# Kernel optimization log

Measured on AMD Instinct MI355X. Metric: run time of the kernel, lower is better.

Reference implementation:

```python
import jax, jax.numpy as jnp
import numpy as np

NUM_ROUTING = 3

def _squash(s):
    # squared_norm * s / ((1 + squared_norm) * sqrt(squared_norm)), norm over last dim
    sn = jnp.sum(s * s, axis=-1, keepdims=True)
    return sn * s / ((1.0 + sn) * jnp.sqrt(sn))

def setup_inputs() -> dict:
    key = jax.random.key(0)
    kx, kw = jax.random.split(key)
    B, IN_CAPS, IN_DIM, OUT_CAPS, OUT_DIM = 64, 8192, 8, 8, 16
    x = jax.random.normal(kx, (B, IN_CAPS, IN_DIM), dtype=jnp.float32)
    W = 0.01 * jax.random.normal(kw, (IN_CAPS, OUT_CAPS, IN_DIM, OUT_DIM), dtype=jnp.float32)
    return {"x": x, "W": W}

def reference(x, W):
    # x: [B, in_caps, in_dim]; W: [in_caps, out_caps, in_dim, out_dim]
    u_hat = jnp.einsum('ijnm,bin->bijm', W, x)          # [B, i, j, m]
    temp_u_hat = jax.lax.stop_gradient(u_hat)           # detach, routing uses no grads
    B, I, J = x.shape[0], W.shape[0], W.shape[1]
    b = jnp.zeros((B, I, J), dtype=x.dtype)
    for _ in range(NUM_ROUTING - 1):
        c = jax.nn.softmax(b, axis=2)                   # over out_caps j
        s = jnp.einsum('bij,bijm->bjm', c, temp_u_hat)  # [B, j, m]
        v = _squash(s)
        b = b + jnp.einsum('bjm,bijm->bij', v, temp_u_hat)  # agreement
    c = jax.nn.softmax(b, axis=2)
    s = jnp.einsum('bij,bijm->bjm', c, u_hat)
    return _squash(s)                                   # [B, out_caps, out_dim]
```

## Files before the change

kernel.cpp:

```cpp
#include <hip/hip_runtime.h>


#define BB      64
#define ICAPS   8192
#define NDIM    8
#define JCAPS   8
#define MDIM    16
#define NBLK    256
#define ICHUNK  (ICAPS / NBLK)
#define IG      8
#define NSTAGE  (ICHUNK / IG)
#define JW      4
#define MW      4
#define WJ_STRIDE (NDIM * MDIM + 4)
#define WI_STRIDE (JCAPS * WJ_STRIDE)
#define S_ELEMS  (BB * JCAPS * MDIM)

template <int MODE>
__global__ __launch_bounds__(512, 1) void caps_pass_kernel(
    const float* __restrict__ x, const float* __restrict__ W,
    const float* __restrict__ vsum, float* __restrict__ partial)
{
    __shared__ float Wlds[IG * WI_STRIDE];

    const int tid = threadIdx.x;
    const int b   = tid >> 3;
    const int g   = tid & 7;
    const int jh  = g >> 2;
    const int mq  = g & 3;
    const int blk = blockIdx.x;
    const int i0  = blk * ICHUNK;

    float s_acc[JW][MW];
    #pragma unroll
    for (int a = 0; a < JW; ++a)
        #pragma unroll
        for (int c = 0; c < MW; ++c) s_acc[a][c] = 0.f;

    float vreg[JW][MW];
    if (MODE == 1) {
        #pragma unroll
        for (int jj = 0; jj < JW; ++jj) {
            const float4 vv = *(const float4*)&vsum[(b * JCAPS + jh * JW + jj) * MDIM + mq * 4];
            vreg[jj][0] = vv.x; vreg[jj][1] = vv.y; vreg[jj][2] = vv.z; vreg[jj][3] = vv.w;
        }
    }

    for (int st = 0; st < NSTAGE; ++st) {
        {
            const int iL  = tid >> 6;
            const int rem = tid & 63;
            const int j   = rem >> 3;
            const int n   = rem & 7;
            const float4* src = (const float4*)(W + (size_t)(i0 + st * IG + iL) * 1024
                                                  + j * 128 + n * 16);
            float4* dst = (float4*)&Wlds[iL * WI_STRIDE + j * WJ_STRIDE + n * 16];
            dst[0] = src[0]; dst[1] = src[1]; dst[2] = src[2]; dst[3] = src[3];
        }
        __syncthreads();

        #pragma unroll
        for (int ii = 0; ii < IG; ++ii) {
            const int i = i0 + st * IG + ii;
            const float4 xa = *(const float4*)&x[((size_t)b * ICAPS + i) * NDIM];
            const float4 xb = *(const float4*)&x[((size_t)b * ICAPS + i) * NDIM + 4];
            const float xs[8] = {xa.x, xa.y, xa.z, xa.w, xb.x, xb.y, xb.z, xb.w};

            float u[JW][MW] = {};
            const float* wbase = &Wlds[ii * WI_STRIDE + (jh * JW) * WJ_STRIDE + mq * 4];
            #pragma unroll
            for (int jj = 0; jj < JW; ++jj) {
                #pragma unroll
                for (int n = 0; n < NDIM; ++n) {
                    const float4 wq = *(const float4*)&wbase[jj * WJ_STRIDE + n * MDIM];
                    u[jj][0] += xs[n] * wq.x;
                    u[jj][1] += xs[n] * wq.y;
                    u[jj][2] += xs[n] * wq.z;
                    u[jj][3] += xs[n] * wq.w;
                }
            }

            if (MODE == 0) {
                #pragma unroll
                for (int jj = 0; jj < JW; ++jj)
                    #pragma unroll
                    for (int mm = 0; mm < MW; ++mm) s_acc[jj][mm] += u[jj][mm];
            } else {
                float lp[JW];
                #pragma unroll
                for (int jj = 0; jj < JW; ++jj)
                    lp[jj] = u[jj][0] * vreg[jj][0] + u[jj][1] * vreg[jj][1]
                           + u[jj][2] * vreg[jj][2] + u[jj][3] * vreg[jj][3];
                #pragma unroll
                for (int jj = 0; jj < JW; ++jj) {
                    lp[jj] += __shfl_xor(lp[jj], 1);
                    lp[jj] += __shfl_xor(lp[jj], 2);
                }
                float lo[JW];
                #pragma unroll
                for (int jj = 0; jj < JW; ++jj) lo[jj] = __shfl_xor(lp[jj], 4);
                float mx = lp[0];
                #pragma unroll
                for (int jj = 1; jj < JW; ++jj) mx = fmaxf(mx, lp[jj]);
                #pragma unroll
                for (int jj = 0; jj < JW; ++jj) mx = fmaxf(mx, lo[jj]);
                float e[JW];
                float den = 0.f;
                #pragma unroll
                for (int jj = 0; jj < JW; ++jj) {
                    e[jj] = __expf(lp[jj] - mx);
                    den += e[jj];
                    den += __expf(lo[jj] - mx);
                }
                const float inv = 1.0f / den;
                #pragma unroll
                for (int jj = 0; jj < JW; ++jj) {
                    const float c = e[jj] * inv;
                    #pragma unroll
                    for (int mm = 0; mm < MW; ++mm) s_acc[jj][mm] += c * u[jj][mm];
                }
            }
        }
        __syncthreads();
    }

    const float sc = (MODE == 0) ? 0.125f : 1.0f;
    float* pp = partial + (size_t)blk * S_ELEMS + b * (JCAPS * MDIM);
    #pragma unroll
    for (int jj = 0; jj < JW; ++jj) {
        float4 o;
        o.x = s_acc[jj][0] * sc; o.y = s_acc[jj][1] * sc;
        o.z = s_acc[jj][2] * sc; o.w = s_acc[jj][3] * sc;
        *(float4*)&pp[(jh * JW + jj) * MDIM + mq * 4] = o;
    }
}

template <int FINAL>
__global__ __launch_bounds__(256) void caps_reduce_kernel(
    const float* __restrict__ partial, float* __restrict__ vsum, float* __restrict__ out)
{
    __shared__ float sd[256];
    const int bo  = blockIdx.x;
    const int tid = threadIdx.x;
    const int tl  = tid >> 3;
    const int kg  = tid & 7;
    const int t   = bo * 32 + tl;

    float ssum = 0.f;
    const float* p = partial + (size_t)kg * 32 * S_ELEMS + t;
    #pragma unroll
    for (int k = 0; k < 32; ++k) ssum += p[(size_t)k * S_ELEMS];
    sd[tid] = ssum;
    __syncthreads();

    if (tid < 32) {
        const int tt = bo * 32 + tid;
        float s = 0.f;
        #pragma unroll
        for (int q = 0; q < 8; ++q) s += sd[tid * 8 + q];
        float sn = s * s;
        sn += __shfl_xor(sn, 1);
        sn += __shfl_xor(sn, 2);
        sn += __shfl_xor(sn, 4);
        sn += __shfl_xor(sn, 8);
        const float v = s * sqrtf(sn) / (1.f + sn);
        if (FINAL) out[tt] = v;
        else       vsum[tt] += v;
    }
}

extern "C" void kernel_launch(void* const* d_in, const int* in_sizes, int n_in,
                              void* d_out, int out_size, void* d_ws, size_t ws_size,
                              hipStream_t stream)
{
    const float* x = (const float*)d_in[0];
    const float* W = (const float*)d_in[1];
    float* out = (float*)d_out;

    float* partial = (float*)d_ws;
    float* vsum    = partial + (size_t)NBLK * S_ELEMS;

    hipMemsetAsync(vsum, 0, S_ELEMS * sizeof(float), stream);

    caps_pass_kernel<0><<<NBLK, 512, 0, stream>>>(x, W, vsum, partial);
    caps_reduce_kernel<0><<<256, 256, 0, stream>>>(partial, vsum, nullptr);
    caps_pass_kernel<1><<<NBLK, 512, 0, stream>>>(x, W, vsum, partial);
    caps_reduce_kernel<0><<<256, 256, 0, stream>>>(partial, vsum, nullptr);
    caps_pass_kernel<1><<<NBLK, 512, 0, stream>>>(x, W, vsum, partial);
    caps_reduce_kernel<1><<<256, 256, 0, stream>>>(partial, vsum, out);
}
```

Before: 224.2 us.

## Remap pass kernel threads to one j per thread with two batches each

The pass kernel moves from 512 to 1024 threads per block. Each thread now owns one output capsule j and two batch rows, instead of four j's for one batch row, so the softmax over j becomes a cross-lane shuffle reduction. The max-subtraction is dropped, and the reciprocal is replaced with a fast rcp intrinsic. The reduce kernel is reshaped to 64 outputs per block, and the first reduce now writes vsum directly, which removes the memset. This spreads the work across more waves, but each thread still reloads x for its two rows, and removing the max-subtraction risks exp overflow if the logits get large.

```diff
diff --git a/kernel.cpp b/kernel.cpp
--- a/kernel.cpp
+++ b/kernel.cpp
@@ -10,162 +10,137 @@
 #define ICHUNK  (ICAPS / NBLK)
 #define IG      8
 #define NSTAGE  (ICHUNK / IG)
-#define JW      4
-#define MW      4
 #define WJ_STRIDE (NDIM * MDIM + 4)
 #define WI_STRIDE (JCAPS * WJ_STRIDE)
 #define S_ELEMS  (BB * JCAPS * MDIM)
 
 template <int MODE>
-__global__ __launch_bounds__(512, 1) void caps_pass_kernel(
+__global__ __launch_bounds__(1024, 4) void caps_pass_kernel(
     const float* __restrict__ x, const float* __restrict__ W,
     const float* __restrict__ vsum, float* __restrict__ partial)
 {
     __shared__ float Wlds[IG * WI_STRIDE];
 
     const int tid = threadIdx.x;
-    const int b   = tid >> 3;
-    const int g   = tid & 7;
-    const int jh  = g >> 2;
-    const int mq  = g & 3;
+    const int mq  = tid & 3;
+    const int j   = (tid >> 2) & 7;
+    const int bg  = tid >> 5;
+    const int b0  = bg;
+    const int b1  = bg + 32;
     const int blk = blockIdx.x;
     const int i0  = blk * ICHUNK;
 
-    float s_acc[JW][MW];
-    #pragma unroll
-    for (int a = 0; a < JW; ++a)
-        #pragma unroll
-        for (int c = 0; c < MW; ++c) s_acc[a][c] = 0.f;
+    float s0[4] = {0.f, 0.f, 0.f, 0.f};
+    float s1[4] = {0.f, 0.f, 0.f, 0.f};
 
-    float vreg[JW][MW];
+    float v0[4], v1[4];
     if (MODE == 1) {
-        #pragma unroll
-        for (int jj = 0; jj < JW; ++jj) {
-            const float4 vv = *(const float4*)&vsum[(b * JCAPS + jh * JW + jj) * MDIM + mq * 4];
-            vreg[jj][0] = vv.x; vreg[jj][1] = vv.y; vreg[jj][2] = vv.z; vreg[jj][3] = vv.w;
-        }
+        const float4 a = *(const float4*)&vsum[(b0 * JCAPS + j) * MDIM + mq * 4];
+        v0[0] = a.x; v0[1] = a.y; v0[2] = a.z; v0[3] = a.w;
+        const float4 c = *(const float4*)&vsum[(b1 * JCAPS + j) * MDIM + mq * 4];
+        v1[0] = c.x; v1[1] = c.y; v1[2] = c.z; v1[3] = c.w;
     }
 
     for (int st = 0; st < NSTAGE; ++st) {
         {
-            const int iL  = tid >> 6;
-            const int rem = tid & 63;
-            const int j   = rem >> 3;
-            const int n   = rem & 7;
+            const int iL  = tid >> 7;
+            const int rem = tid & 127;
             const float4* src = (const float4*)(W + (size_t)(i0 + st * IG + iL) * 1024
-                                                  + j * 128 + n * 16);
-            float4* dst = (float4*)&Wlds[iL * WI_STRIDE + j * WJ_STRIDE + n * 16];
-            dst[0] = src[0]; dst[1] = src[1]; dst[2] = src[2]; dst[3] = src[3];
+                                                  + rem * 8);
+            float4* dst = (float4*)&Wlds[iL * WI_STRIDE + (rem >> 4) * WJ_STRIDE
+                                         + (rem & 15) * 8];
+            dst[0] = src[0]; dst[1] = src[1];
         }
         __syncthreads();
 
         #pragma unroll
         for (int ii = 0; ii < IG; ++ii) {
             const int i = i0 + st * IG + ii;
-            const float4 xa = *(const float4*)&x[((size_t)b * ICAPS + i) * NDIM];
-            const float4 xb = *(const float4*)&x[((size_t)b * ICAPS + i) * NDIM + 4];
-            const float xs[8] = {xa.x, xa.y, xa.z, xa.w, xb.x, xb.y, xb.z, xb.w};
+            const float4 xa0 = *(const float4*)&x[((size_t)b0 * ICAPS + i) * NDIM];
+            const float4 xb0 = *(const float4*)&x[((size_t)b0 * ICAPS + i) * NDIM + 4];
+            const float4 xa1 = *(const float4*)&x[((size_t)b1 * ICAPS + i) * NDIM];
+            const float4 xb1 = *(const float4*)&x[((size_t)b1 * ICAPS + i) * NDIM + 4];
+            const float xs0[8] = {xa0.x, xa0.y, xa0.z, xa0.w, xb0.x, xb0.y, xb0.z, xb0.w};
+            const float xs1[8] = {xa1.x, xa1.y, xa1.z, xa1.w, xb1.x, xb1.y, xb1.z, xb1.w};
 
-            float u[JW][MW] = {};
-            const float* wbase = &Wlds[ii * WI_STRIDE + (jh * JW) * WJ_STRIDE + mq * 4];
+            float u0[4] = {0.f, 0.f, 0.f, 0.f};
+            float u1[4] = {0.f, 0.f, 0.f, 0.f};
+            const float* wb = &Wlds[ii * WI_STRIDE + j * WJ_STRIDE + mq * 4];
             #pragma unroll
-            for (int jj = 0; jj < JW; ++jj) {
-                #pragma unroll
-                for (int n = 0; n < NDIM; ++n) {
-                    const float4 wq = *(const float4*)&wbase[jj * WJ_STRIDE + n * MDIM];
-                    u[jj][0] += xs[n] * wq.x;
-                    u[jj][1] += xs[n] * wq.y;
-                    u[jj][2] += xs[n] * wq.z;
-                    u[jj][3] += xs[n] * wq.w;
-                }
+            for (int n = 0; n < NDIM; ++n) {
+                const float4 wq = *(const float4*)&wb[n * MDIM];
+                u0[0] += xs0[n] * wq.x; u0[1] += xs0[n] * wq.y;
+                u0[2] += xs0[n] * wq.z; u0[3] += xs0[n] * wq.w;
+                u1[0] += xs1[n] * wq.x; u1[1] += xs1[n] * wq.y;
+                u1[2] += xs1[n] * wq.z; u1[3] += xs1[n] * wq.w;
             }
 
             if (MODE == 0) {
                 #pragma unroll
-                for (int jj = 0; jj < JW; ++jj)
-                    #pragma unroll
-                    for (int mm = 0; mm < MW; ++mm) s_acc[jj][mm] += u[jj][mm];
+                for (int m = 0; m < 4; ++m) { s0[m] += u0[m]; s1[m] += u1[m]; }
             } else {
-                float lp[JW];
+                float lp0 = u0[0] * v0[0] + u0[1] * v0[1] + u0[2] * v0[2] + u0[3] * v0[3];
+                float lp1 = u1[0] * v1[0] + u1[1] * v1[1] + u1[2] * v1[2] + u1[3] * v1[3];
+                lp0 += __shfl_xor(lp0, 1);  lp0 += __shfl_xor(lp0, 2);
+                lp1 += __shfl_xor(lp1, 1);  lp1 += __shfl_xor(lp1, 2);
+                const float e0 = __expf(lp0);
+                const float e1 = __expf(lp1);
+                float d0 = e0, d1 = e1;
+                d0 += __shfl_xor(d0, 4); d0 += __shfl_xor(d0, 8); d0 += __shfl_xor(d0, 16);
+                d1 += __shfl_xor(d1, 4); d1 += __shfl_xor(d1, 8); d1 += __shfl_xor(d1, 16);
+                const float c0 = e0 * __builtin_amdgcn_rcpf(d0);
+                const float c1 = e1 * __builtin_amdgcn_rcpf(d1);
                 #pragma unroll
-                for (int jj = 0; jj < JW; ++jj)
-                    lp[jj] = u[jj][0] * vreg[jj][0] + u[jj][1] * vreg[jj][1]
-                           + u[jj][2] * vreg[jj][2] + u[jj][3] * vreg[jj][3];
-                #pragma unroll
-                for (int jj = 0; jj < JW; ++jj) {
-                    lp[jj] += __shfl_xor(lp[jj], 1);
-                    lp[jj] += __shfl_xor(lp[jj], 2);
-                }
-                float lo[JW];
-                #pragma unroll
-                for (int jj = 0; jj < JW; ++jj) lo[jj] = __shfl_xor(lp[jj], 4);
-                float mx = lp[0];
-                #pragma unroll
-                for (int jj = 1; jj < JW; ++jj) mx = fmaxf(mx, lp[jj]);
-                #pragma unroll
-                for (int jj = 0; jj < JW; ++jj) mx = fmaxf(mx, lo[jj]);
-                float e[JW];
-                float den = 0.f;
-                #pragma unroll
-                for (int jj = 0; jj < JW; ++jj) {
-                    e[jj] = __expf(lp[jj] - mx);
-                    den += e[jj];
-                    den += __expf(lo[jj] - mx);
-                }
-                const float inv = 1.0f / den;
-                #pragma unroll
-                for (int jj = 0; jj < JW; ++jj) {
-                    const float c = e[jj] * inv;
-                    #pragma unroll
-                    for (int mm = 0; mm < MW; ++mm) s_acc[jj][mm] += c * u[jj][mm];
-                }
+                for (int m = 0; m < 4; ++m) { s0[m] += c0 * u0[m]; s1[m] += c1 * u1[m]; }
             }
         }
         __syncthreads();
     }
 
     const float sc = (MODE == 0) ? 0.125f : 1.0f;
-    float* pp = partial + (size_t)blk * S_ELEMS + b * (JCAPS * MDIM);
-    #pragma unroll
-    for (int jj = 0; jj < JW; ++jj) {
-        float4 o;
-        o.x = s_acc[jj][0] * sc; o.y = s_acc[jj][1] * sc;
-        o.z = s_acc[jj][2] * sc; o.w = s_acc[jj][3] * sc;
-        *(float4*)&pp[(jh * JW + jj) * MDIM + mq * 4] = o;
-    }
+    float* pp = partial + (size_t)blk * S_ELEMS;
+    float4 o0, o1;
+    o0.x = s0[0] * sc; o0.y = s0[1] * sc; o0.z = s0[2] * sc; o0.w = s0[3] * sc;
+    o1.x = s1[0] * sc; o1.y = s1[1] * sc; o1.z = s1[2] * sc; o1.w = s1[3] * sc;
+    *(float4*)&pp[(b0 * JCAPS + j) * MDIM + mq * 4] = o0;
+    *(float4*)&pp[(b1 * JCAPS + j) * MDIM + mq * 4] = o1;
 }
 
-template <int FINAL>
+template <int OP>
 __global__ __launch_bounds__(256) void caps_reduce_kernel(
     const float* __restrict__ partial, float* __restrict__ vsum, float* __restrict__ out)
 {
     __shared__ float sd[256];
     const int bo  = blockIdx.x;
     const int tid = threadIdx.x;
-    const int tl  = tid >> 3;
-    const int kg  = tid & 7;
-    const int t   = bo * 32 + tl;
+    const int kg  = tid >> 6;
+    const int tl  = tid & 63;
+    const int t   = bo * 64 + tl;
 
-    float ssum = 0.f;
-    const float* p = partial + (size_t)kg * 32 * S_ELEMS + t;
+    float a0 = 0.f, a1 = 0.f, a2 = 0.f, a3 = 0.f;
+    const float* p = partial + (size_t)kg * 64 * S_ELEMS + t;
     #pragma unroll
-    for (int k = 0; k < 32; ++k) ssum += p[(size_t)k * S_ELEMS];
-    sd[tid] = ssum;
+    for (int k = 0; k < 64; k += 4) {
+        a0 += p[(size_t)(k + 0) * S_ELEMS];
+        a1 += p[(size_t)(k + 1) * S_ELEMS];
+        a2 += p[(size_t)(k + 2) * S_ELEMS];
+        a3 += p[(size_t)(k + 3) * S_ELEMS];
+    }
+    sd[tid] = (a0 + a1) + (a2 + a3);
     __syncthreads();
 
-    if (tid < 32) {
-        const int tt = bo * 32 + tid;
-        float s = 0.f;
-        #pragma unroll
-        for (int q = 0; q < 8; ++q) s += sd[tid * 8 + q];
+    if (tid < 64) {
+        const float s = (sd[tid] + sd[64 + tid]) + (sd[128 + tid] + sd[192 + tid]);
         float sn = s * s;
         sn += __shfl_xor(sn, 1);
         sn += __shfl_xor(sn, 2);
         sn += __shfl_xor(sn, 4);
         sn += __shfl_xor(sn, 8);
         const float v = s * sqrtf(sn) / (1.f + sn);
-        if (FINAL) out[tt] = v;
-        else       vsum[tt] += v;
+        const int tt = bo * 64 + tid;
+        if (OP == 2)      out[tt]   = v;
+        else if (OP == 1) vsum[tt] += v;
+        else              vsum[tt]  = v;
     }
 }
 
@@ -180,12 +155,10 @@
     float* partial = (float*)d_ws;
     float* vsum    = partial + (size_t)NBLK * S_ELEMS;
 
-    hipMemsetAsync(vsum, 0, S_ELEMS * sizeof(float), stream);
-
-    caps_pass_kernel<0><<<NBLK, 512, 0, stream>>>(x, W, vsum, partial);
-    caps_reduce_kernel<0><<<256, 256, 0, stream>>>(partial, vsum, nullptr);
-    caps_pass_kernel<1><<<NBLK, 512, 0, stream>>>(x, W, vsum, partial);
-    caps_reduce_kernel<0><<<256, 256, 0, stream>>>(partial, vsum, nullptr);
-    caps_pass_kernel<1><<<NBLK, 512, 0, stream>>>(x, W, vsum, partial);
-    caps_reduce_kernel<1><<<256, 256, 0, stream>>>(partial, vsum, out);
+    caps_pass_kernel<0><<<NBLK, 1024, 0, stream>>>(x, W, vsum, partial);
+    caps_reduce_kernel<0><<<128, 256, 0, stream>>>(partial, vsum, nullptr);
+    caps_pass_kernel<1><<<NBLK, 1024, 0, stream>>>(x, W, vsum, partial);
+    caps_reduce_kernel<1><<<128, 256, 0, stream>>>(partial, vsum, nullptr);
+    caps_pass_kernel<1><<<NBLK, 1024, 0, stream>>>(x, W, vsum, partial);
+    caps_reduce_kernel<2><<<128, 256, 0, stream>>>(partial, vsum, out);
 }
```

New measurement: 207.0 us. 7.7% less time.
